# Kernel optimization log

Measured on AMD Instinct MI355X. Metric: run time of the kernel, lower is better.

Reference implementation:

```python
import jax, jax.numpy as jnp
import numpy as np

KEEP_RATIO = 0.25
BLOCK = 8
TEMP = 0.1


def setup_inputs() -> dict:
    key = jax.random.key(0)
    features = jax.random.normal(key, (8, 256, 132, 132), dtype=jnp.float32)
    return {"features": features, "enabled": 1}


def reference(features, enabled):
    B, C, H, W = features.shape
    if not enabled:
        return jnp.ones((B, C, H, W), dtype=features.dtype)
    # pad H, W up to multiples of BLOCK (zeros, like F.pad default)
    ph = (-H) % BLOCK
    pw = (-W) % BLOCK
    x = jnp.pad(jnp.abs(features), ((0, 0), (0, 0), (0, ph), (0, pw)))
    Hp, Wp = H + ph, W + pw
    nh, nw = Hp // BLOCK, Wp // BLOCK
    # avg_pool2d(kernel=stride=BLOCK) == block-mean via reshape
    pooled = x.reshape(B, C, nh, BLOCK, nw, BLOCK).mean(axis=(3, 5))  # [B,C,nh,nw]
    total = nh * nw
    scores = pooled.reshape(B, C, total)
    keep = max(1, min(total, int(round(total * KEEP_RATIO))))
    top_vals, top_idx = jax.lax.top_k(scores, keep)  # sorted descending, like torch.topk
    # hard mask: scatter ones at topk indices
    flat_idx = top_idx.reshape(B * C, keep)
    hard = (jnp.zeros((B * C, total), dtype=features.dtype)
            .at[jnp.arange(B * C)[:, None], flat_idx].set(1.0)
            .reshape(B, C, total))
    # training-mode straight-through soft blend
    thr = jax.lax.stop_gradient(top_vals[..., -1:])  # kth value as threshold
    soft = jax.nn.sigmoid((scores - thr) / TEMP)
    soft = soft * (keep / jnp.maximum(soft.sum(-1, keepdims=True), 1e-6))
    soft = jnp.clip(soft, 0.0, 1.0)
    mask = jax.lax.stop_gradient(hard) - jax.lax.stop_gradient(soft) + soft
    # upsample blocks back to pixels (repeat_interleave) and crop padding
    block_mask = mask.reshape(B, C, nh, nw)
    full = jnp.repeat(jnp.repeat(block_mask, BLOCK, axis=2), BLOCK, axis=3)
    return full[:, :, :H, :W]
```

## Files before the change

### kernel.cpp

```cpp
#include <hip/hip_runtime.h>


#define HH 132
#define WW 132
#define NB 17
#define TOTAL 289
#define KEEP 72
#define NTHREADS 256

__global__ __launch_bounds__(NTHREADS)
void gate_kernel(const float* __restrict__ feats,
                 const int* __restrict__ enabled_p,
                 float* __restrict__ out) {
    const int plane = blockIdx.x;
    const int t = threadIdx.x;
    const float* __restrict__ fp = feats + (size_t)plane * (HH * WW);
    float* __restrict__ op = out + (size_t)plane * (HH * WW);

    __shared__ double s_col[WW];
    __shared__ double s_score[TOTAL];
    __shared__ float  s_hard[TOTAL];

    for (int br = 0; br < NB; ++br) {
        const int r0 = br * 8;
        const int nr = (r0 + 8 <= HH) ? 8 : (HH - r0);
        if (t < WW) {
            double acc = 0.0;
            const float* rp = fp + (size_t)r0 * WW + t;
            #pragma unroll
            for (int k = 0; k < 8; ++k) {
                if (k < nr) acc += (double)fabsf(rp[k * WW]);
            }
            s_col[t] = acc;
        }
        __syncthreads();
        if (t < NB) {
            const int c0 = t * 8;
            const int nc = (c0 + 8 <= WW) ? 8 : (WW - c0);
            double s = 0.0;
            for (int j = 0; j < nc; ++j) s += s_col[c0 + j];
            s_score[br * NB + t] = s;
        }
        __syncthreads();
    }

    const int en = *enabled_p;
    for (int i = t; i < TOTAL; i += NTHREADS) {
        const double si = s_score[i];
        int rank = 0;
        for (int j = 0; j < TOTAL; ++j) {
            const double sj = s_score[j];
            rank += (int)((sj > si) || ((sj == si) && (j < i)));
        }
        s_hard[i] = (!en || rank < KEEP) ? 1.0f : 0.0f;
    }
    __syncthreads();

    constexpr int NV = (HH * WW) / 4;
    float4* __restrict__ op4 = (float4*)op;
    for (int v = t; v < NV; v += NTHREADS) {
        const int base = v * 4;
        const int row = base / WW;
        const int col = base - row * WW;
        const float m = s_hard[(row >> 3) * NB + (col >> 3)];
        op4[v] = make_float4(m, m, m, m);
    }
}

extern "C" void kernel_launch(void* const* d_in, const int* in_sizes, int n_in,
                              void* d_out, int out_size, void* d_ws, size_t ws_size,
                              hipStream_t stream) {
    const float* feats = (const float*)d_in[0];
    const int* enabled = (const int*)d_in[1];
    float* out = (float*)d_out;
    const int planes = 8 * 256;
    gate_kernel<<<planes, NTHREADS, 0, stream>>>(feats, enabled, out);
}
```

Before: 269.4 us.

## Stream plane with float4 loads and LDS atomic block accumulation

Replaces the 17-step row-band pooling loop, which had two barriers per band and used only 132 threads, with one pass over the plane. Each thread loads float4 vectors and adds their absolute sum into the per-block score using shared-memory double atomics. The rank loop now reads scores as double2 pairs, and the mask output uses nontemporal stores. Double atomics in LDS may be slow and make the summation order nondeterministic, so scores that tie or nearly tie could rank differently.

Result: faster. 260.4 us (-3.4%).

```diff
diff --git a/kernel.cpp b/kernel.cpp
--- a/kernel.cpp
+++ b/kernel.cpp
@@ -7,72 +7,69 @@
 #define TOTAL 289
 #define KEEP 72
 #define NTHREADS 256
+#define NV ((HH * WW) / 4)
+
+typedef float floatx4 __attribute__((ext_vector_type(4)));
 
 __global__ __launch_bounds__(NTHREADS)
-void gate_kernel(const float* __restrict__ feats,
+void gate_kernel(const float4* __restrict__ feats4,
                  const int* __restrict__ enabled_p,
-                 float* __restrict__ out) {
+                 float4* __restrict__ out4) {
     const int plane = blockIdx.x;
     const int t = threadIdx.x;
-    const float* __restrict__ fp = feats + (size_t)plane * (HH * WW);
-    float* __restrict__ op = out + (size_t)plane * (HH * WW);
+    const float4* __restrict__ fp = feats4 + (size_t)plane * NV;
+    floatx4* __restrict__ op = (floatx4*)(out4 + (size_t)plane * NV);
 
-    __shared__ double s_col[WW];
-    __shared__ double s_score[TOTAL];
-    __shared__ float  s_hard[TOTAL];
+    __shared__ __align__(16) double s_score[TOTAL + 1];
+    __shared__ float s_hard[TOTAL];
 
-    for (int br = 0; br < NB; ++br) {
-        const int r0 = br * 8;
-        const int nr = (r0 + 8 <= HH) ? 8 : (HH - r0);
-        if (t < WW) {
-            double acc = 0.0;
-            const float* rp = fp + (size_t)r0 * WW + t;
-            #pragma unroll
-            for (int k = 0; k < 8; ++k) {
-                if (k < nr) acc += (double)fabsf(rp[k * WW]);
-            }
-            s_col[t] = acc;
-        }
-        __syncthreads();
-        if (t < NB) {
-            const int c0 = t * 8;
-            const int nc = (c0 + 8 <= WW) ? 8 : (WW - c0);
-            double s = 0.0;
-            for (int j = 0; j < nc; ++j) s += s_col[c0 + j];
-            s_score[br * NB + t] = s;
-        }
-        __syncthreads();
+    for (int i = t; i < TOTAL + 1; i += NTHREADS)
+        s_score[i] = (i < TOTAL) ? 0.0 : -1.0e300;
+    __syncthreads();
+
+    for (int v = t; v < NV; v += NTHREADS) {
+        const float4 x = fp[v];
+        const double s = (double)fabsf(x.x) + (double)fabsf(x.y)
+                       + (double)fabsf(x.z) + (double)fabsf(x.w);
+        const int base = v * 4;
+        const int row = base / WW;
+        const int col = base - row * WW;
+        atomicAdd(&s_score[(row >> 3) * NB + (col >> 3)], s);
     }
+    __syncthreads();
 
     const int en = *enabled_p;
+    const double2* __restrict__ sc2 = (const double2*)s_score;
     for (int i = t; i < TOTAL; i += NTHREADS) {
         const double si = s_score[i];
         int rank = 0;
-        for (int j = 0; j < TOTAL; ++j) {
-            const double sj = s_score[j];
-            rank += (int)((sj > si) || ((sj == si) && (j < i)));
+        #pragma unroll 5
+        for (int q = 0; q < (TOTAL + 1) / 2; ++q) {
+            const double2 sj = sc2[q];
+            const int j = q * 2;
+            rank += (int)((sj.x > si) || ((sj.x == si) && (j < i)));
+            rank += (int)((sj.y > si) || ((sj.y == si) && (j + 1 < i)));
         }
         s_hard[i] = (!en || rank < KEEP) ? 1.0f : 0.0f;
     }
     __syncthreads();
 
-    constexpr int NV = (HH * WW) / 4;
-    float4* __restrict__ op4 = (float4*)op;
     for (int v = t; v < NV; v += NTHREADS) {
         const int base = v * 4;
         const int row = base / WW;
         const int col = base - row * WW;
         const float m = s_hard[(row >> 3) * NB + (col >> 3)];
-        op4[v] = make_float4(m, m, m, m);
+        const floatx4 mv = {m, m, m, m};
+        __builtin_nontemporal_store(mv, &op[v]);
     }
 }
 
 extern "C" void kernel_launch(void* const* d_in, const int* in_sizes, int n_in,
                               void* d_out, int out_size, void* d_ws, size_t ws_size,
                               hipStream_t stream) {
-    const float* feats = (const float*)d_in[0];
+    const float4* feats = (const float4*)d_in[0];
     const int* enabled = (const int*)d_in[1];
-    float* out = (float*)d_out;
+    float4* out = (float4*)d_out;
     const int planes = 8 * 256;
     gate_kernel<<<planes, NTHREADS, 0, stream>>>(feats, enabled, out);
 }
```
